# Performance work log

Measured on AMD Instinct MI355X. Metric: run time of the kernel, lower is better.

## Reference

```python
import jax, jax.numpy as jnp
import numpy as np

Q_HEADS, KV_HEADS, DIMS = 16, 4, 1024
HEAD_DIM = DIMS // Q_HEADS          # 64
GROUPS = Q_HEADS // KV_HEADS        # 4
ROPE_BASE = 10000.0


def rope(x):
    # x: (..., s, d) -- standard interleaved rotary embedding, base 10000
    s, d = x.shape[-2], x.shape[-1]
    inv_freq = 1.0 / (ROPE_BASE ** (jnp.arange(0, d, 2, dtype=jnp.float32) / d))
    ang = jnp.arange(s, dtype=jnp.float32)[:, None] * inv_freq[None, :]  # (s, d/2)
    cos, sin = jnp.cos(ang), jnp.sin(ang)
    x1, x2 = x[..., 0::2], x[..., 1::2]
    out = jnp.stack([x1 * cos - x2 * sin, x1 * sin + x2 * cos], axis=-1)
    return out.reshape(x.shape).astype(x.dtype)


def setup_inputs() -> dict:
    key = jax.random.key(0)
    k1, k2, k3, k4, k5, k6 = jax.random.split(key, 6)
    B, S, E = 4, 2048, 1024
    q = jax.random.normal(k1, (B, S, E), dtype=jnp.float32)
    kv = jax.random.normal(k2, (B, S, E), dtype=jnp.float32)
    sc = 1.0 / np.sqrt(E)
    Wq = jax.random.normal(k3, (E, Q_HEADS, HEAD_DIM), dtype=jnp.float32) * sc
    Wk = jax.random.normal(k4, (E, KV_HEADS, HEAD_DIM), dtype=jnp.float32) * sc
    Wv = jax.random.normal(k5, (E, KV_HEADS, HEAD_DIM), dtype=jnp.float32) * sc
    Wo = jax.random.normal(k6, (HEAD_DIM, E), dtype=jnp.float32) / np.sqrt(HEAD_DIM)
    return {"q": q, "kv": kv, "Wq": Wq, "Wk": Wk, "Wv": Wv, "Wo": Wo}


def reference(q, kv, Wq, Wk, Wv, Wo):
    B, S, E = q.shape
    qh = jnp.einsum('bse,ehd->bshd', q, Wq)    # (B,S,Q_HEADS,hd)
    kh = jnp.einsum('bse,ehd->bshd', kv, Wk)   # (B,S,KV_HEADS,hd)
    vh = jnp.einsum('bse,ehd->bshd', kv, Wv)
    # rearrange '... s (h g) d -> ... g h s d' with g=GROUPS (h = KV_HEADS outer)
    qh = qh.reshape(B, S, KV_HEADS, GROUPS, HEAD_DIM).transpose(0, 3, 2, 1, 4)  # (B,g,h,S,d)
    kh = kh.transpose(0, 2, 1, 3)  # (B,h,S,d)
    vh = vh.transpose(0, 2, 1, 3)  # (B,h,S,d)
    qh = rope(qh)
    kh = rope(kh)
    # NOTE: sums over group axis g (faithful to original einsum)
    scores = jnp.einsum('bghsd,bhad->bhsa', qh, kh)
    attn = jax.nn.softmax(scores / (HEAD_DIM ** 0.5), axis=-1)
    out = jnp.einsum('bhsa,bhad->bhsd', attn, vh)  # (B,h,S,d)
    out = out.mean(axis=1)                          # mean over kv heads -> (B,S,d)
    return out @ Wo                                 # (B,S,E)
```

## Files before the change

### kernel.cpp

```cpp
#include <hip/hip_runtime.h>
#include <math.h>

#define SS 2048
#define EE 1024

using bf16x8 = __attribute__((ext_vector_type(8))) short;
using f32x4  = __attribute__((ext_vector_type(4))) float;

__device__ inline short f2bf(float x) {
    unsigned u = __builtin_bit_cast(unsigned, x);
    return (short)((u + 0x7fffu + ((u >> 16) & 1u)) >> 16);
}
__device__ inline short f2bf_r(float x) {
    return (short)((__builtin_bit_cast(unsigned, x) + 0x8000u) >> 16);
}
__device__ inline unsigned pk_bf16(float a, float b) {
    unsigned ua = __builtin_bit_cast(unsigned, a) + 0x8000u;
    unsigned ub = __builtin_bit_cast(unsigned, b) + 0x8000u;
    return __builtin_amdgcn_perm(ub, ua, 0x07060302u);
}

__global__ __launch_bounds__(256) void prep_weights(const float* __restrict__ Wq,
                                                    const float* __restrict__ Wk,
                                                    const float* __restrict__ Wv,
                                                    const float* __restrict__ Wo,
                                                    short* __restrict__ Wall,
                                                    short* __restrict__ Wo4,
                                                    float2* __restrict__ RT) {
    int idx = blockIdx.x * 256 + threadIdx.x;
    int c = idx >> 10, e = idx & 1023;
    int h = c >> 6, d = c & 63;
    const float* p = Wq + (size_t)e * 1024 + h * 256 + d;
    Wall[(size_t)c * 1024 + e] = f2bf(0.18033688011112042f * (p[0] + p[64] + p[128] + p[192]));
    Wall[(size_t)(256 + c) * 1024 + e] = f2bf(Wk[(size_t)e * 256 + c]);
    Wall[(size_t)(512 + c) * 1024 + e] = f2bf(Wv[(size_t)e * 256 + c]);
    Wo4[(size_t)e * 256 + c] = f2bf(0.25f * Wo[(size_t)d * 1024 + e]);
    if (idx < 65536) {
        int s = idx >> 5, ii = idx & 31;
        float freq = __expf(-(float)ii * (9.210340371976184f / 32.0f));
        float sn, cs;
        sincosf((float)s * freq, &sn, &cs);
        RT[idx] = (float2){cs, sn};
    }
}

__global__ __launch_bounds__(256) void proj_kernel(const float* __restrict__ q,
                                                   const float* __restrict__ kv,
                                                   const short* __restrict__ Wall,
                                                   const float2* __restrict__ RT,
                                                   short* __restrict__ Qb,
                                                   short* __restrict__ Kb,
                                                   short* __restrict__ Vt) {
    __shared__ alignas(16) short As[64][72];
    __shared__ alignas(16) short Bs[64][72];
    int tid = threadIdx.x;
    int wave = tid >> 6, lane = tid & 63, quad = lane >> 4, c16 = lane & 15;
    int m0 = blockIdx.x * 64, n0 = blockIdx.y * 64;
    const float* A = (n0 < 256) ? q : kv;

    f32x4 acc[4];
    #pragma unroll
    for (int j = 0; j < 4; j++) acc[j] = (f32x4){0.f, 0.f, 0.f, 0.f};

    for (int k0 = 0; k0 < 1024; k0 += 64) {
        #pragma unroll
        for (int i = 0; i < 4; i++) {
            int id = i * 256 + tid, r = id >> 4, ch = id & 15;
            float4 v = *(const float4*)&A[(size_t)(m0 + r) * 1024 + k0 + ch * 4];
            uint2 u;
            u.x = pk_bf16(v.x, v.y);
            u.y = pk_bf16(v.z, v.w);
            *(uint2*)&As[r][ch * 4] = u;
        }
        #pragma unroll
        for (int i = 0; i < 2; i++) {
            int id = i * 256 + tid, r = id >> 3, ch = id & 7;
            *(int4*)&Bs[r][ch * 8] =
                *(const int4*)&Wall[(size_t)(n0 + r) * 1024 + k0 + ch * 8];
        }
        __syncthreads();
        #pragma unroll
        for (int ks = 0; ks < 64; ks += 32) {
            bf16x8 af = *(const bf16x8*)&As[wave * 16 + c16][ks + quad * 8];
            #pragma unroll
            for (int nt = 0; nt < 4; nt++) {
                bf16x8 bfr = *(const bf16x8*)&Bs[nt * 16 + c16][ks + quad * 8];
                acc[nt] = __builtin_amdgcn_mfma_f32_16x16x32_bf16(af, bfr, acc[nt], 0, 0, 0);
            }
        }
        __syncthreads();
    }
    if (n0 < 512) {
        #pragma unroll
        for (int nt = 0; nt < 4; nt++) {
            int cl = nt * 16 + c16;
            int ii = cl >> 1;
            float sgn = (lane & 1) ? 1.0f : -1.0f;
            f32x4 v = acc[nt];
            #pragma unroll
            for (int r = 0; r < 4; r++) {
                int rl = wave * 16 + quad * 4 + r;
                float2 cs = RT[((m0 + rl) & (SS - 1)) * 32 + ii];
                float other = __shfl_xor(v[r], 1);
                As[rl][cl] = f2bf_r(v[r] * cs.x + sgn * cs.y * other);
            }
        }
        __syncthreads();
        short* dstb = (n0 < 256) ? Qb : Kb;
        int nc0 = n0 & 255;
        #pragma unroll
        for (int i = 0; i < 2; i++) {
            int id = i * 256 + tid, r = id >> 3, ch = id & 7;
            *(int4*)&dstb[(size_t)(m0 + r) * 256 + nc0 + ch * 8] =
                *(const int4*)&As[r][ch * 8];
        }
    } else {
        short (*Lt)[72] = As;
        #pragma unroll
        for (int nt = 0; nt < 4; nt++) {
            int cl = nt * 16 + c16;
            int sl = wave * 16 + quad * 4;
            f32x4 v = acc[nt];
            uint2 u;
            u.x = pk_bf16(v[0], v[1]);
            u.y = pk_bf16(v[2], v[3]);
            *(uint2*)&Lt[cl][sl] = u;
        }
        __syncthreads();
        int b = m0 >> 11, s0 = m0 & (SS - 1), c0 = n0 - 512;
        #pragma unroll
        for (int i = 0; i < 2; i++) {
            int id = i * 256 + tid, c = id >> 3, ch = id & 7;
            *(int4*)&Vt[((size_t)(b * 256 + c0 + c)) * SS + s0 + ch * 8] =
                *(const int4*)&Lt[c][ch * 8];
        }
    }
}

__global__ __launch_bounds__(512, 4) void attn_kernel(const short* __restrict__ Qb,
                                                      const short* __restrict__ Kb,
                                                      const short* __restrict__ Vt,
                                                      short* __restrict__ Ob) {
    __shared__ alignas(16) short Qs[64][72];
    __shared__ alignas(16) short Ps2[64][72];
    __shared__ alignas(16) short Ks[2][64][72];
    __shared__ alignas(16) short Vs[2][64][72];
    int tid = threadIdx.x;
    int wave = tid >> 6, lane = tid & 63, quad = lane >> 4, c16 = lane & 15;
    int rq = wave & 3, kh = wave >> 2;
    int qt = blockIdx.x, bh = blockIdx.y;
    int q0 = qt * 64;
    size_t qkbase = (size_t)(bh >> 2) * SS * 256 + (bh & 3) * 64;
    size_t vtbase = (size_t)(bh * 64) * SS;

    {
        int r = tid >> 3, ch = tid & 7;
        *(int4*)&Qs[r][ch * 8] = *(const int4*)&Qb[qkbase + (size_t)(q0 + r) * 256 + ch * 8];
    }
    __syncthreads();
    bf16x8 aq0 = *(const bf16x8*)&Qs[rq * 16 + c16][quad * 8];
    bf16x8 aq1 = *(const bf16x8*)&Qs[rq * 16 + c16][32 + quad * 8];
    short (*Ps)[72] = (kh == 0) ? (short (*)[72])Qs[rq * 16] : (short (*)[72])Ps2[rq * 16];

    float lsum[4] = {0.f, 0.f, 0.f, 0.f};
    f32x4 o[4];
    #pragma unroll
    for (int dt = 0; dt < 4; dt++) o[dt] = (f32x4){0.f, 0.f, 0.f, 0.f};

    int sr = tid >> 3, sch = tid & 7;
    int4 kr0 = *(const int4*)&Kb[qkbase + (size_t)sr * 256 + sch * 8];
    int4 kr1 = *(const int4*)&Kb[qkbase + (size_t)(1024 + sr) * 256 + sch * 8];
    int4 vr0 = *(const int4*)&Vt[vtbase + (size_t)sr * SS + sch * 8];
    int4 vr1 = *(const int4*)&Vt[vtbase + (size_t)sr * SS + 1024 + sch * 8];

    for (int kt = 0; kt < 16; kt++) {
        __syncthreads();
        *(int4*)&Ks[0][sr][sch * 8] = kr0;
        *(int4*)&Ks[1][sr][sch * 8] = kr1;
        *(int4*)&Vs[0][sr][sch * 8] = vr0;
        *(int4*)&Vs[1][sr][sch * 8] = vr1;
        if (kt < 15) {
            int a1 = (kt + 1) * 64;
            kr0 = *(const int4*)&Kb[qkbase + (size_t)(a1 + sr) * 256 + sch * 8];
            kr1 = *(const int4*)&Kb[qkbase + (size_t)(1024 + a1 + sr) * 256 + sch * 8];
            vr0 = *(const int4*)&Vt[vtbase + (size_t)sr * SS + a1 + sch * 8];
            vr1 = *(const int4*)&Vt[vtbase + (size_t)sr * SS + 1024 + a1 + sch * 8];
        }
        __syncthreads();
        f32x4 sv[4];
        #pragma unroll
        for (int nt = 0; nt < 4; nt++) sv[nt] = (f32x4){0.f, 0.f, 0.f, 0.f};
        #pragma unroll
        for (int nt = 0; nt < 4; nt++) {
            bf16x8 bk0 = *(const bf16x8*)&Ks[kh][nt * 16 + c16][quad * 8];
            bf16x8 bk1 = *(const bf16x8*)&Ks[kh][nt * 16 + c16][32 + quad * 8];
            sv[nt] = __builtin_amdgcn_mfma_f32_16x16x32_bf16(aq0, bk0, sv[nt], 0, 0, 0);
            sv[nt] = __builtin_amdgcn_mfma_f32_16x16x32_bf16(aq1, bk1, sv[nt], 0, 0, 0);
        }
        #pragma unroll
        for (int nt = 0; nt < 4; nt++)
            #pragma unroll
            for (int r = 0; r < 4; r++) sv[nt][r] = __builtin_exp2f(sv[nt][r]);
        #pragma unroll
        for (int r = 0; r < 4; r++)
            lsum[r] += (sv[0][r] + sv[1][r]) + (sv[2][r] + sv[3][r]);
        #pragma unroll
        for (int nt = 0; nt < 4; nt++)
            #pragma unroll
            for (int r = 0; r < 4; r++)
                Ps[quad * 4 + r][nt * 16 + c16] = f2bf_r(sv[nt][r]);
        #pragma unroll
        for (int ks = 0; ks < 64; ks += 32) {
            bf16x8 ap = *(const bf16x8*)&Ps[c16][ks + quad * 8];
            #pragma unroll
            for (int dt = 0; dt < 4; dt++) {
                bf16x8 bv = *(const bf16x8*)&Vs[kh][dt * 16 + c16][ks + quad * 8];
                o[dt] = __builtin_amdgcn_mfma_f32_16x16x32_bf16(ap, bv, o[dt], 0, 0, 0);
            }
        }
    }
    #pragma unroll
    for (int off = 1; off < 16; off <<= 1)
        #pragma unroll
        for (int r = 0; r < 4; r++) lsum[r] += __shfl_xor(lsum[r], off);

    __syncthreads();
    float (*Ox)[68] = (float (*)[68])&Ks[0][0][0];
    float* Lx = (float*)&Vs[0][0][0];
    short (*Ot)[72] = (short (*)[72])&Vs[1][0][0];
    int base = rq * 16 + quad * 4;
    if (wave >= 4) {
        #pragma unroll
        for (int dt = 0; dt < 4; dt++)
            #pragma unroll
            for (int r = 0; r < 4; r++)
                Ox[base + r][dt * 16 + c16] = o[dt][r];
        if (c16 == 0)
            #pragma unroll
            for (int r = 0; r < 4; r++) Lx[base + r] = lsum[r];
    }
    __syncthreads();
    if (wave < 4) {
        #pragma unroll
        for (int r = 0; r < 4; r++) {
            float rl = __builtin_amdgcn_rcpf(lsum[r] + Lx[base + r]);
            #pragma unroll
            for (int dt = 0; dt < 4; dt++)
                Ot[base + r][dt * 16 + c16] =
                    f2bf_r((o[dt][r] + Ox[base + r][dt * 16 + c16]) * rl);
        }
    }
    __syncthreads();
    {
        int r = tid >> 3, ch = tid & 7;
        int b = bh >> 2, h = bh & 3;
        *(int4*)&Ob[((size_t)(b * SS + q0 + r)) * 256 + h * 64 + ch * 8] =
            *(const int4*)&Ot[r][ch * 8];
    }
}

__global__ __launch_bounds__(256) void outproj_kernel(const short* __restrict__ Ob,
                                                      const short* __restrict__ Wo4,
                                                      float* __restrict__ out) {
    __shared__ alignas(16) short As[128][72];
    __shared__ alignas(16) short Bs[64][72];
    int tid = threadIdx.x;
    int wave = tid >> 6, lane = tid & 63, quad = lane >> 4, c16 = lane & 15;
    int m0 = blockIdx.x * 128, n0 = blockIdx.y * 64;

    f32x4 acc[2][4];
    #pragma unroll
    for (int i = 0; i < 2; i++)
        #pragma unroll
        for (int j = 0; j < 4; j++) acc[i][j] = (f32x4){0.f, 0.f, 0.f, 0.f};

    for (int k0 = 0; k0 < 256; k0 += 64) {
        #pragma unroll
        for (int i = 0; i < 4; i++) {
            int id = i * 256 + tid, r = id >> 3, ch = id & 7;
            *(int4*)&As[r][ch * 8] =
                *(const int4*)&Ob[(size_t)(m0 + r) * 256 + k0 + ch * 8];
        }
        #pragma unroll
        for (int i = 0; i < 2; i++) {
            int id = i * 256 + tid, r = id >> 3, ch = id & 7;
            *(int4*)&Bs[r][ch * 8] =
                *(const int4*)&Wo4[(size_t)(n0 + r) * 256 + k0 + ch * 8];
        }
        __syncthreads();
        #pragma unroll
        for (int ks = 0; ks < 64; ks += 32) {
            bf16x8 af[2], bfr[4];
            #pragma unroll
            for (int mt = 0; mt < 2; mt++)
                af[mt] = *(const bf16x8*)&As[wave * 32 + mt * 16 + c16][ks + quad * 8];
            #pragma unroll
            for (int nt = 0; nt < 4; nt++)
                bfr[nt] = *(const bf16x8*)&Bs[nt * 16 + c16][ks + quad * 8];
            #pragma unroll
            for (int mt = 0; mt < 2; mt++)
                #pragma unroll
                for (int nt = 0; nt < 4; nt++)
                    acc[mt][nt] = __builtin_amdgcn_mfma_f32_16x16x32_bf16(
                        af[mt], bfr[nt], acc[mt][nt], 0, 0, 0);
        }
        __syncthreads();
    }
    #pragma unroll
    for (int mt = 0; mt < 2; mt++)
        #pragma unroll
        for (int nt = 0; nt < 4; nt++) {
            int col = n0 + nt * 16 + c16;
            int rowb = m0 + wave * 32 + mt * 16 + quad * 4;
            #pragma unroll
            for (int r = 0; r < 4; r++)
                out[(size_t)(rowb + r) * 1024 + col] = acc[mt][nt][r];
        }
}

extern "C" void kernel_launch(void* const* d_in, const int* in_sizes, int n_in,
                              void* d_out, int out_size, void* d_ws, size_t ws_size,
                              hipStream_t stream) {
    const float* q  = (const float*)d_in[0];
    const float* kv = (const float*)d_in[1];
    const float* Wq = (const float*)d_in[2];
    const float* Wk = (const float*)d_in[3];
    const float* Wv = (const float*)d_in[4];
    const float* Wo = (const float*)d_in[5];
    float* out = (float*)d_out;

    short* Qb    = (short*)d_ws;
    short* Kb    = Qb + 2097152;
    short* Vt    = Kb + 2097152;
    short* Wall  = Vt + 2097152;
    short* Wo4   = Wall + 786432;
    float2* RT   = (float2*)(Wo4 + 262144);
    short* Ob    = (short*)(RT + 65536);

    prep_weights<<<1024, 256, 0, stream>>>(Wq, Wk, Wv, Wo, Wall, Wo4, RT);

    proj_kernel<<<dim3(128, 12), 256, 0, stream>>>(q, kv, Wall, RT, Qb, Kb, Vt);

    attn_kernel<<<dim3(32, 16), 512, 0, stream>>>(Qb, Kb, Vt, Ob);

    outproj_kernel<<<dim3(64, 16), 256, 0, stream>>>(Ob, Wo4, out);
}
```

Baseline: 199.4 us.

## Pre-convert activations to bf16 and use direct global-to-LDS loads with larger projection tiles

Adds a pass in the prep kernel that converts the q and kv activations to bf16 once, so the projection GEMM reads half-width data instead of converting fp32 inside its inner loop. The projection kernel now uses global_load_lds to stream A and B tiles straight into unpadded LDS, and each block computes a 128x64 tile with every wave holding a 4x2 grid of MFMA accumulators. The intent is to cut projection-side memory traffic and VALU conversion work and raise operand reuse. In exchange it adds an extra full write and read of the activations, and the unpadded LDS rows may cause bank conflicts on fragment reads.

```diff
diff --git a/kernel.cpp b/kernel.cpp
--- a/kernel.cpp
+++ b/kernel.cpp
@@ -19,15 +19,37 @@
     unsigned ub = __builtin_bit_cast(unsigned, b) + 0x8000u;
     return __builtin_amdgcn_perm(ub, ua, 0x07060302u);
 }
-
-__global__ __launch_bounds__(256) void prep_weights(const float* __restrict__ Wq,
+__device__ inline void gl16(const short* g, short* l) {
+    __builtin_amdgcn_global_load_lds(
+        (const __attribute__((address_space(1))) void*)g,
+        (__attribute__((address_space(3))) void*)l, 16, 0, 0);
+}
+
+__global__ __launch_bounds__(256) void prep_weights(const float* __restrict__ q,
+                                                    const float* __restrict__ kv,
+                                                    const float* __restrict__ Wq,
                                                     const float* __restrict__ Wk,
                                                     const float* __restrict__ Wv,
                                                     const float* __restrict__ Wo,
+                                                    short* __restrict__ Ab,
                                                     short* __restrict__ Wall,
                                                     short* __restrict__ Wo4,
                                                     float2* __restrict__ RT) {
-    int idx = blockIdx.x * 256 + threadIdx.x;
+    if (blockIdx.x < 8192) {
+        int gt = blockIdx.x * 256 + threadIdx.x;
+        size_t e0 = (size_t)gt * 8;
+        const float* src = (e0 < 8388608) ? (q + e0) : (kv + (e0 - 8388608));
+        float4 v0 = *(const float4*)src;
+        float4 v1 = *(const float4*)(src + 4);
+        int4 u;
+        u.x = pk_bf16(v0.x, v0.y);
+        u.y = pk_bf16(v0.z, v0.w);
+        u.z = pk_bf16(v1.x, v1.y);
+        u.w = pk_bf16(v1.z, v1.w);
+        *(int4*)&Ab[e0] = u;
+        return;
+    }
+    int idx = (blockIdx.x - 8192) * 256 + threadIdx.x;
     int c = idx >> 10, e = idx & 1023;
     int h = c >> 6, d = c & 63;
     const float* p = Wq + (size_t)e * 1024 + h * 256 + d;
@@ -44,93 +66,108 @@
     }
 }
 
-__global__ __launch_bounds__(256) void proj_kernel(const float* __restrict__ q,
-                                                   const float* __restrict__ kv,
+__global__ __launch_bounds__(256) void proj_kernel(const short* __restrict__ Ab,
                                                    const short* __restrict__ Wall,
                                                    const float2* __restrict__ RT,
                                                    short* __restrict__ Qb,
                                                    short* __restrict__ Kb,
                                                    short* __restrict__ Vt) {
-    __shared__ alignas(16) short As[64][72];
-    __shared__ alignas(16) short Bs[64][72];
+    __shared__ alignas(16) short SMEM[128 * 64 + 64 * 64];
+    short (*As)[64] = (short (*)[64])SMEM;
+    short (*Bs)[64] = (short (*)[64])(SMEM + 128 * 64);
     int tid = threadIdx.x;
     int wave = tid >> 6, lane = tid & 63, quad = lane >> 4, c16 = lane & 15;
-    int m0 = blockIdx.x * 64, n0 = blockIdx.y * 64;
-    const float* A = (n0 < 256) ? q : kv;
-
-    f32x4 acc[4];
-    #pragma unroll
-    for (int j = 0; j < 4; j++) acc[j] = (f32x4){0.f, 0.f, 0.f, 0.f};
+    int wm = wave >> 1, wn = wave & 1;
+    int m0 = blockIdx.x * 128, n0 = blockIdx.y * 64;
+    const short* A = Ab + ((n0 < 256) ? 0 : (size_t)8388608);
+
+    int lr = lane >> 3, lc = lane & 7;
+    f32x4 acc[4][2];
+    #pragma unroll
+    for (int i = 0; i < 4; i++)
+        #pragma unroll
+        for (int j = 0; j < 2; j++) acc[i][j] = (f32x4){0.f, 0.f, 0.f, 0.f};
 
     for (int k0 = 0; k0 < 1024; k0 += 64) {
+        __syncthreads();
         #pragma unroll
         for (int i = 0; i < 4; i++) {
-            int id = i * 256 + tid, r = id >> 4, ch = id & 15;
-            float4 v = *(const float4*)&A[(size_t)(m0 + r) * 1024 + k0 + ch * 4];
-            uint2 u;
-            u.x = pk_bf16(v.x, v.y);
-            u.y = pk_bf16(v.z, v.w);
-            *(uint2*)&As[r][ch * 4] = u;
+            int seg = wave * 4 + i;
+            int r = seg * 8 + lr;
+            gl16(&A[(size_t)(m0 + r) * 1024 + k0 + lc * 8], &As[seg * 8][0]);
         }
         #pragma unroll
         for (int i = 0; i < 2; i++) {
-            int id = i * 256 + tid, r = id >> 3, ch = id & 7;
-            *(int4*)&Bs[r][ch * 8] =
-                *(const int4*)&Wall[(size_t)(n0 + r) * 1024 + k0 + ch * 8];
+            int seg = wave * 2 + i;
+            int r = seg * 8 + lr;
+            gl16(&Wall[(size_t)(n0 + r) * 1024 + k0 + lc * 8], &Bs[seg * 8][0]);
         }
         __syncthreads();
         #pragma unroll
         for (int ks = 0; ks < 64; ks += 32) {
-            bf16x8 af = *(const bf16x8*)&As[wave * 16 + c16][ks + quad * 8];
-            #pragma unroll
-            for (int nt = 0; nt < 4; nt++) {
-                bf16x8 bfr = *(const bf16x8*)&Bs[nt * 16 + c16][ks + quad * 8];
-                acc[nt] = __builtin_amdgcn_mfma_f32_16x16x32_bf16(af, bfr, acc[nt], 0, 0, 0);
-            }
-        }
-        __syncthreads();
-    }
+            bf16x8 af[4], bfr[2];
+            #pragma unroll
+            for (int mt = 0; mt < 4; mt++)
+                af[mt] = *(const bf16x8*)&As[wm * 64 + mt * 16 + c16][ks + quad * 8];
+            #pragma unroll
+            for (int nt = 0; nt < 2; nt++)
+                bfr[nt] = *(const bf16x8*)&Bs[wn * 32 + nt * 16 + c16][ks + quad * 8];
+            #pragma unroll
+            for (int mt = 0; mt < 4; mt++)
+                #pragma unroll
+                for (int nt = 0; nt < 2; nt++)
+                    acc[mt][nt] = __builtin_amdgcn_mfma_f32_16x16x32_bf16(
+                        af[mt], bfr[nt], acc[mt][nt], 0, 0, 0);
+        }
+    }
+    __syncthreads();
     if (n0 < 512) {
         #pragma unroll
-        for (int nt = 0; nt < 4; nt++) {
-            int cl = nt * 16 + c16;
-            int ii = cl >> 1;
-            float sgn = (lane & 1) ? 1.0f : -1.0f;
-            f32x4 v = acc[nt];
-            #pragma unroll
-            for (int r = 0; r < 4; r++) {
-                int rl = wave * 16 + quad * 4 + r;
-                float2 cs = RT[((m0 + rl) & (SS - 1)) * 32 + ii];
-                float other = __shfl_xor(v[r], 1);
-                As[rl][cl] = f2bf_r(v[r] * cs.x + sgn * cs.y * other);
+        for (int mt = 0; mt < 4; mt++) {
+            #pragma unroll
+            for (int nt = 0; nt < 2; nt++) {
+                int cl = wn * 32 + nt * 16 + c16;
+                int ii = cl >> 1;
+                float sgn = (lane & 1) ? 1.0f : -1.0f;
+                f32x4 v = acc[mt][nt];
+                #pragma unroll
+                for (int r = 0; r < 4; r++) {
+                    int rl = wm * 64 + mt * 16 + quad * 4 + r;
+                    float2 cs = RT[((m0 + rl) & (SS - 1)) * 32 + ii];
+                    float other = __shfl_xor(v[r], 1);
+                    As[rl][cl] = f2bf_r(v[r] * cs.x + sgn * cs.y * other);
+                }
             }
         }
         __syncthreads();
         short* dstb = (n0 < 256) ? Qb : Kb;
         int nc0 = n0 & 255;
         #pragma unroll
-        for (int i = 0; i < 2; i++) {
+        for (int i = 0; i < 4; i++) {
             int id = i * 256 + tid, r = id >> 3, ch = id & 7;
             *(int4*)&dstb[(size_t)(m0 + r) * 256 + nc0 + ch * 8] =
                 *(const int4*)&As[r][ch * 8];
         }
     } else {
-        short (*Lt)[72] = As;
-        #pragma unroll
-        for (int nt = 0; nt < 4; nt++) {
-            int cl = nt * 16 + c16;
-            int sl = wave * 16 + quad * 4;
-            f32x4 v = acc[nt];
-            uint2 u;
-            u.x = pk_bf16(v[0], v[1]);
-            u.y = pk_bf16(v[2], v[3]);
-            *(uint2*)&Lt[cl][sl] = u;
+        short (*Lt)[136] = (short(*)[136])SMEM;
+        #pragma unroll
+        for (int mt = 0; mt < 4; mt++) {
+            #pragma unroll
+            for (int nt = 0; nt < 2; nt++) {
+                int cl = wn * 32 + nt * 16 + c16;
+                int sl = wm * 64 + mt * 16 + quad * 4;
+                f32x4 v = acc[mt][nt];
+                uint2 u;
+                u.x = pk_bf16(v[0], v[1]);
+                u.y = pk_bf16(v[2], v[3]);
+                *(uint2*)&Lt[cl][sl] = u;
+            }
         }
         __syncthreads();
         int b = m0 >> 11, s0 = m0 & (SS - 1), c0 = n0 - 512;
         #pragma unroll
-        for (int i = 0; i < 2; i++) {
-            int id = i * 256 + tid, c = id >> 3, ch = id & 7;
+        for (int i = 0; i < 4; i++) {
+            int id = i * 256 + tid, c = id >> 4, ch = id & 15;
             *(int4*)&Vt[((size_t)(b * 256 + c0 + c)) * SS + s0 + ch * 8] =
                 *(const int4*)&Lt[c][ch * 8];
         }
@@ -336,10 +373,11 @@
     short* Wo4   = Wall + 786432;
     float2* RT   = (float2*)(Wo4 + 262144);
     short* Ob    = (short*)(RT + 65536);
-
-    prep_weights<<<1024, 256, 0, stream>>>(Wq, Wk, Wv, Wo, Wall, Wo4, RT);
-
-    proj_kernel<<<dim3(128, 12), 256, 0, stream>>>(q, kv, Wall, RT, Qb, Kb, Vt);
+    short* Ab    = Ob + 2097152;
+
+    prep_weights<<<9216, 256, 0, stream>>>(q, kv, Wq, Wk, Wv, Wo, Ab, Wall, Wo4, RT);
+
+    proj_kernel<<<dim3(64, 12), 256, 0, stream>>>(Ab, Wall, RT, Qb, Kb, Vt);
 
     attn_kernel<<<dim3(32, 16), 512, 0, stream>>>(Qb, Kb, Vt, Ob);
 
```

After: 194.5 us. 1.03x faster.
